# Kernel optimization log

Hardware: AMD Instinct MI355X
Metric: run time of the kernel (lower is better)

## Reference

```python
import jax, jax.numpy as jnp
import numpy as np

TAU = 0.28
EPS = 1e-08

def _l2norm(x):
    # F.normalize(dim=1): x / max(||x||, 1e-12)
    n = jnp.sqrt(jnp.sum(x * x, axis=1, keepdims=True))
    return x / jnp.maximum(n, 1e-12)

def setup_inputs() -> dict:
    key = jax.random.key(0)
    k1, k2 = jax.random.split(key)
    N, D = 16384, 64
    return {
        "user_embed": jax.random.normal(k1, (N, D), dtype=jnp.float32),
        "pos_item_embed": jax.random.normal(k2, (N, D), dtype=jnp.float32),
    }

def reference(user_embed, pos_item_embed):
    u = _l2norm(user_embed)          # [N, D]
    i = _l2norm(pos_item_embed)      # [N, D]
    pos_score = jnp.exp(jnp.sum(u * i, axis=-1) / TAU)          # [N]
    ui = jnp.matmul(u, i.T)          # [N, N]
    uu = jnp.matmul(u, u.T)          # [N, N]
    total = jnp.sum(jnp.exp((ui + uu) / TAU), axis=1)           # [N]
    na_loss = -jnp.log(pos_score / (total + EPS))
    return jnp.mean(na_loss)
```

## Files before the change

kernel.cpp:

```cpp
#include <hip/hip_runtime.h>
#include <hip/hip_bf16.h>

#define NROWS 16384
#define DIM 64
#define BCOLS 512
#define BROWS 1024
#define NCS (NROWS / BCOLS)
#define NRG (NROWS / BROWS)

static constexpr float TAU = 0.28f;
static constexpr float EPS = 1e-8f;
static constexpr float EXP2_SCALE = (float)(1.0 / (0.28 * 0.6931471805599453));
static constexpr float LN2F = 0.69314718055994530942f;

using short8 = __attribute__((ext_vector_type(8))) short;
using f32x4  = __attribute__((ext_vector_type(4))) float;

typedef __attribute__((address_space(1))) const unsigned char ga_t;
typedef __attribute__((address_space(3))) unsigned char la_t;

__global__ __launch_bounds__(256) void prep_kernel(
    const float* __restrict__ u, const float* __restrict__ v,
    __hip_bfloat16* __restrict__ a_out, __hip_bfloat16* __restrict__ w_out,
    float* __restrict__ p_out, float* __restrict__ total, float* __restrict__ out)
{
    const int lane = threadIdx.x & 63;
    const int wv   = threadIdx.x >> 6;
    const int row  = blockIdx.x * 4 + wv;

    const float uu = u[row * DIM + lane];
    const float ii = v[row * DIM + lane];
    float su = uu * uu, si = ii * ii, sd = uu * ii;
#pragma unroll
    for (int m = 1; m < 64; m <<= 1) {
        su += __shfl_xor(su, m, 64);
        si += __shfl_xor(si, m, 64);
        sd += __shfl_xor(sd, m, 64);
    }
    const float inv_u = 1.0f / fmaxf(sqrtf(su), 1e-12f);
    const float inv_i = 1.0f / fmaxf(sqrtf(si), 1e-12f);
    const float un = uu * inv_u;
    const float in = ii * inv_i;
    a_out[row * DIM + lane] = __float2bfloat16(EXP2_SCALE * un);
    w_out[row * DIM + lane] = __float2bfloat16(un + in);
    if (lane == 0) {
        p_out[row] = sd * inv_u * inv_i * (1.0f / TAU);
        total[row] = 0.0f;
    }
    if (blockIdx.x == 0 && threadIdx.x == 0) out[0] = 0.0f;
}

__global__ __launch_bounds__(512, 4) void score_kernel(
    const __hip_bfloat16* __restrict__ A, const __hip_bfloat16* __restrict__ W,
    float* __restrict__ total)
{
    __shared__ alignas(16) ushort blds[BCOLS * DIM];

    const int tid  = threadIdx.x;
    const int lane = tid & 63;
    const int wv   = tid >> 6;
    const int l15  = lane & 15;
    const int quad = lane >> 4;
    const int cs   = blockIdx.x & (NCS - 1);
    const int rg   = blockIdx.x >> 5;
    const int col0    = cs * BCOLS;
    const int rowbase = rg * BROWS;

    const ushort* Au = (const ushort*)A;
    const ushort* Wu = (const ushort*)W;

#pragma unroll
    for (int q = 0; q < 8; q++) {
        const int p = q * 512 + tid;
        const int j = p >> 3;
        const int c = (p & 7) ^ (j & 7);
        const ushort* g = Wu + (size_t)(col0 + j) * DIM + c * 8;
        __builtin_amdgcn_global_load_lds((ga_t*)g, (la_t*)&blds[(size_t)p * 8], 16, 0, 0);
    }
    __syncthreads();

    for (int si = 0; si < 4; si++) {
        const int r0 = rowbase + wv * 128 + si * 32;

        short8 af[2][2];
#pragma unroll
        for (int rs = 0; rs < 2; rs++)
#pragma unroll
            for (int kk = 0; kk < 2; kk++)
                af[rs][kk] = *(const short8*)(
                    Au + (size_t)(r0 + rs * 16 + l15) * DIM + kk * 32 + quad * 8);

        float rowsum[2][4];
#pragma unroll
        for (int rs = 0; rs < 2; rs++)
#pragma unroll
            for (int r = 0; r < 4; r++) rowsum[rs][r] = 0.0f;

#pragma unroll 8
        for (int ct = 0; ct < BCOLS / 16; ct++) {
            const int jl = ct * 16 + l15;
            const int sw = l15 & 7;
            const short8 b0 = *(const short8*)&blds[(size_t)(jl * 8 + (quad ^ sw)) * 8];
            const short8 b1 = *(const short8*)&blds[(size_t)(jl * 8 + ((4 + quad) ^ sw)) * 8];
#pragma unroll
            for (int rs = 0; rs < 2; rs++) {
                f32x4 acc = {0.f, 0.f, 0.f, 0.f};
                acc = __builtin_amdgcn_mfma_f32_16x16x32_bf16(af[rs][0], b0, acc, 0, 0, 0);
                acc = __builtin_amdgcn_mfma_f32_16x16x32_bf16(af[rs][1], b1, acc, 0, 0, 0);
#pragma unroll
                for (int r = 0; r < 4; r++)
                    rowsum[rs][r] += __builtin_amdgcn_exp2f(acc[r]);
            }
        }

#pragma unroll
        for (int m = 1; m < 16; m <<= 1)
#pragma unroll
            for (int rs = 0; rs < 2; rs++)
#pragma unroll
                for (int r = 0; r < 4; r++)
                    rowsum[rs][r] += __shfl_xor(rowsum[rs][r], m, 64);

        if (l15 == 0) {
#pragma unroll
            for (int rs = 0; rs < 2; rs++)
#pragma unroll
                for (int r = 0; r < 4; r++)
                    atomicAdd(&total[r0 + rs * 16 + quad * 4 + r], rowsum[rs][r]);
        }
    }
}

__global__ __launch_bounds__(256) void finalize_kernel(
    const float* __restrict__ total, const float* __restrict__ p,
    float* __restrict__ out)
{
    __shared__ float red[4];
    const int idx = blockIdx.x * 256 + threadIdx.x;
    float s = __log2f(total[idx] + EPS) * LN2F - p[idx];
#pragma unroll
    for (int m = 1; m < 64; m <<= 1) s += __shfl_xor(s, m, 64);
    if ((threadIdx.x & 63) == 0) red[threadIdx.x >> 6] = s;
    __syncthreads();
    if (threadIdx.x == 0)
        atomicAdd(out, (red[0] + red[1] + red[2] + red[3]) * (1.0f / (float)NROWS));
}

extern "C" void kernel_launch(void* const* d_in, const int* in_sizes, int n_in,
                              void* d_out, int out_size, void* d_ws, size_t ws_size,
                              hipStream_t stream) {
    const float* u = (const float*)d_in[0];
    const float* v = (const float*)d_in[1];

    char* ws = (char*)d_ws;
    __hip_bfloat16* a = (__hip_bfloat16*)(ws);
    __hip_bfloat16* w = (__hip_bfloat16*)(ws + (size_t)NROWS * DIM * 2);
    float* p   = (float*)(ws + (size_t)NROWS * DIM * 4);
    float* tot = (float*)(ws + (size_t)NROWS * DIM * 4 + (size_t)NROWS * 4);

    prep_kernel<<<NROWS / 4, 256, 0, stream>>>(u, v, a, w, p, tot, (float*)d_out);
    score_kernel<<<NRG * NCS, 512, 0, stream>>>(a, w, tot);
    finalize_kernel<<<NROWS / 256, 256, 0, stream>>>(tot, p, (float*)d_out);
}
```

Before: 103.1 us.

## Widen per-wave row tile to 64 rows and vectorize prep kernel loads

The score kernel now has each wave process 64 rows per iteration (four 16-row MFMA tiles) instead of 32. Each B fragment read from LDS is therefore reused across twice as many MFMAs, halving LDS traffic per flop, at the cost of more registers for A fragments and row sums. The prep kernel handles 4 rows per wave with float4 loads and 4-wide bf16 stores, which cuts the launch count and the shuffle-reduction depth.

```diff
diff --git a/kernel.cpp b/kernel.cpp
--- a/kernel.cpp
+++ b/kernel.cpp
@@ -13,8 +13,9 @@
 static constexpr float EXP2_SCALE = (float)(1.0 / (0.28 * 0.6931471805599453));
 static constexpr float LN2F = 0.69314718055994530942f;
 
-using short8 = __attribute__((ext_vector_type(8))) short;
-using f32x4  = __attribute__((ext_vector_type(4))) float;
+using short8  = __attribute__((ext_vector_type(8))) short;
+using f32x4   = __attribute__((ext_vector_type(4))) float;
+using ushort4v = __attribute__((ext_vector_type(4))) unsigned short;
 
 typedef __attribute__((address_space(1))) const unsigned char ga_t;
 typedef __attribute__((address_space(3))) unsigned char la_t;
@@ -26,24 +27,36 @@
 {
     const int lane = threadIdx.x & 63;
     const int wv   = threadIdx.x >> 6;
-    const int row  = blockIdx.x * 4 + wv;
+    const int l15  = lane & 15;
+    const int row  = blockIdx.x * 16 + wv * 4 + (lane >> 4);
 
-    const float uu = u[row * DIM + lane];
-    const float ii = v[row * DIM + lane];
-    float su = uu * uu, si = ii * ii, sd = uu * ii;
+    const float4 uu = *(const float4*)(u + (size_t)row * DIM + l15 * 4);
+    const float4 vv = *(const float4*)(v + (size_t)row * DIM + l15 * 4);
+
+    float su = uu.x * uu.x + uu.y * uu.y + uu.z * uu.z + uu.w * uu.w;
+    float si = vv.x * vv.x + vv.y * vv.y + vv.z * vv.z + vv.w * vv.w;
+    float sd = uu.x * vv.x + uu.y * vv.y + uu.z * vv.z + uu.w * vv.w;
 #pragma unroll
-    for (int m = 1; m < 64; m <<= 1) {
+    for (int m = 1; m < 16; m <<= 1) {
         su += __shfl_xor(su, m, 64);
         si += __shfl_xor(si, m, 64);
         sd += __shfl_xor(sd, m, 64);
     }
     const float inv_u = 1.0f / fmaxf(sqrtf(su), 1e-12f);
     const float inv_i = 1.0f / fmaxf(sqrtf(si), 1e-12f);
-    const float un = uu * inv_u;
-    const float in = ii * inv_i;
-    a_out[row * DIM + lane] = __float2bfloat16(EXP2_SCALE * un);
-    w_out[row * DIM + lane] = __float2bfloat16(un + in);
-    if (lane == 0) {
+
+    alignas(8) __hip_bfloat16 a4[4], w4[4];
+    const float un[4] = {uu.x * inv_u, uu.y * inv_u, uu.z * inv_u, uu.w * inv_u};
+    const float in[4] = {vv.x * inv_i, vv.y * inv_i, vv.z * inv_i, vv.w * inv_i};
+#pragma unroll
+    for (int r = 0; r < 4; r++) {
+        a4[r] = __float2bfloat16(EXP2_SCALE * un[r]);
+        w4[r] = __float2bfloat16(un[r] + in[r]);
+    }
+    *(ushort4v*)((unsigned short*)a_out + (size_t)row * DIM + l15 * 4) = *(ushort4v*)a4;
+    *(ushort4v*)((unsigned short*)w_out + (size_t)row * DIM + l15 * 4) = *(ushort4v*)w4;
+
+    if (l15 == 0) {
         p_out[row] = sd * inv_u * inv_i * (1.0f / TAU);
         total[row] = 0.0f;
     }
@@ -79,51 +92,51 @@
     }
     __syncthreads();
 
-    for (int si = 0; si < 4; si++) {
-        const int r0 = rowbase + wv * 128 + si * 32;
+#pragma unroll 1
+    for (int si = 0; si < 2; si++) {
+        const int r0 = rowbase + si * 512 + wv * 64;
 
-        short8 af[2][2];
+        short8 af[4][2];
 #pragma unroll
-        for (int rs = 0; rs < 2; rs++)
+        for (int rs = 0; rs < 4; rs++)
 #pragma unroll
             for (int kk = 0; kk < 2; kk++)
                 af[rs][kk] = *(const short8*)(
                     Au + (size_t)(r0 + rs * 16 + l15) * DIM + kk * 32 + quad * 8);
 
-        float rowsum[2][4];
+        f32x4 rowsum[4];
 #pragma unroll
-        for (int rs = 0; rs < 2; rs++)
-#pragma unroll
-            for (int r = 0; r < 4; r++) rowsum[rs][r] = 0.0f;
+        for (int rs = 0; rs < 4; rs++) rowsum[rs] = {0.f, 0.f, 0.f, 0.f};
 
-#pragma unroll 8
+#pragma unroll 4
         for (int ct = 0; ct < BCOLS / 16; ct++) {
             const int jl = ct * 16 + l15;
             const int sw = l15 & 7;
             const short8 b0 = *(const short8*)&blds[(size_t)(jl * 8 + (quad ^ sw)) * 8];
             const short8 b1 = *(const short8*)&blds[(size_t)(jl * 8 + ((4 + quad) ^ sw)) * 8];
 #pragma unroll
-            for (int rs = 0; rs < 2; rs++) {
+            for (int rs = 0; rs < 4; rs++) {
                 f32x4 acc = {0.f, 0.f, 0.f, 0.f};
                 acc = __builtin_amdgcn_mfma_f32_16x16x32_bf16(af[rs][0], b0, acc, 0, 0, 0);
                 acc = __builtin_amdgcn_mfma_f32_16x16x32_bf16(af[rs][1], b1, acc, 0, 0, 0);
+                f32x4 e;
 #pragma unroll
-                for (int r = 0; r < 4; r++)
-                    rowsum[rs][r] += __builtin_amdgcn_exp2f(acc[r]);
+                for (int r = 0; r < 4; r++) e[r] = __builtin_amdgcn_exp2f(acc[r]);
+                rowsum[rs] += e;
             }
         }
 
 #pragma unroll
         for (int m = 1; m < 16; m <<= 1)
 #pragma unroll
-            for (int rs = 0; rs < 2; rs++)
+            for (int rs = 0; rs < 4; rs++)
 #pragma unroll
                 for (int r = 0; r < 4; r++)
                     rowsum[rs][r] += __shfl_xor(rowsum[rs][r], m, 64);
 
         if (l15 == 0) {
 #pragma unroll
-            for (int rs = 0; rs < 2; rs++)
+            for (int rs = 0; rs < 4; rs++)
 #pragma unroll
                 for (int r = 0; r < 4; r++)
                     atomicAdd(&total[r0 + rs * 16 + quad * 4 + r], rowsum[rs][r]);
@@ -158,7 +171,7 @@
     float* p   = (float*)(ws + (size_t)NROWS * DIM * 4);
     float* tot = (float*)(ws + (size_t)NROWS * DIM * 4 + (size_t)NROWS * 4);
 
-    prep_kernel<<<NROWS / 4, 256, 0, stream>>>(u, v, a, w, p, tot, (float*)d_out);
+    prep_kernel<<<NROWS / 16, 256, 0, stream>>>(u, v, a, w, p, tot, (float*)d_out);
     score_kernel<<<NRG * NCS, 512, 0, stream>>>(a, w, tot);
     finalize_kernel<<<NROWS / 256, 256, 0, stream>>>(tot, p, (float*)d_out);
 }
```

Measured after the change: 104.9 us. About the same (+1.7%).
